# Performance work log

Hardware: AMD Instinct MI355X
Metric: run time of the kernel (lower is better)

The kernel has to match this reference:

```python
import jax, jax.numpy as jnp
import numpy as np

B, S, D, E, H, K = 2, 2048, 1024, 8, 4096, 2


def setup_inputs() -> dict:
    key = jax.random.key(0)
    ks = jax.random.split(key, 8)
    w = lambda i, shape: jax.random.normal(ks[i], shape, jnp.float32) * 0.02
    return {
        "x": jax.random.normal(ks[0], (B, S, D), jnp.float32),
        "noise": jax.random.normal(ks[1], (B, S, E), jnp.float32),
        "Wg": w(2, (E, D)),
        "noise_weight": jnp.zeros((E,), jnp.float32),
        "W1": w(3, (E, D, H)),
        "b1": jnp.zeros((E, H), jnp.float32),
        "W2": w(4, (E, D, H)),
        "b2": jnp.zeros((E, H), jnp.float32),
        "Wp": w(5, (E, H, D)),
        "bp": jnp.zeros((E, D), jnp.float32),
        "k": K,
    }


def reference(x, noise, Wg, noise_weight, W1, b1, W2, b2, Wp, bp, k):
    Bb, Ss, Dd = x.shape
    Ee = Wg.shape[0]
    # --- noisy top-k gate (noisy_std = 1.0) ---
    logits = jnp.einsum('bsd,ed->bse', x, Wg)
    noisy = logits + noise * noise_weight            # [B,S,E]
    vals, idx = jax.lax.top_k(noisy, k)              # [B,S,k]
    oh = jax.nn.one_hot(idx, Ee, dtype=x.dtype)      # [B,S,k,E]
    sel = oh.sum(axis=-2) > 0                        # [B,S,E] selected mask
    scat = (oh * vals[..., None]).sum(axis=-2)       # scatter topk logits
    sparse = jnp.where(sel, scat, -jnp.inf)
    gate = jax.nn.softmax(sparse, axis=-1)           # zero weight off-topk
    # --- dense-equivalent expert compute (gate==0 off top-k => same math as masked dispatch) ---
    xf = x.reshape(Bb * Ss, Dd)                      # [T,D]
    gf = gate.reshape(Bb * Ss, Ee)                   # [T,E]
    h1 = jnp.einsum('td,edh->eth', xf, W1) + b1[:, None, :]
    h2 = jnp.einsum('td,edh->eth', xf, W2) + b2[:, None, :]
    hh = h1 * jax.nn.silu(h2)                        # SwiGLU
    outs = jnp.einsum('eth,ehd->etd', hh, Wp) + bp[:, None, :]
    final = jnp.einsum('etd,te->td', outs, gf).reshape(Bb, Ss, Dd)
    return final, idx
```

## Files before the change

kernel.cpp:

```cpp
#include <hip/hip_runtime.h>
#include <math.h>

#define Bc 2
#define Sc 2048
#define Dc 1024
#define Ec 8
#define Hc 4096
#define Tc (Bc*Sc)
#define NSLOT (Tc*2)
#define SLOTPAD 8448
#define FINAL_N ((size_t)Tc*Dc)
#define PROWS ((size_t)SLOTPAD*32)

typedef float f32x4 __attribute__((ext_vector_type(4)));
typedef __bf16 bf16x8 __attribute__((ext_vector_type(8)));

__device__ __forceinline__ unsigned short f2bf(float f) {
    union { float f; unsigned int u; } v; v.f = f;
    return (unsigned short)((v.u + 0x7fffu + ((v.u >> 16) & 1u)) >> 16);
}
__device__ __forceinline__ unsigned int pack2bf(float a, float b) {
    return (unsigned int)f2bf(a) | ((unsigned int)f2bf(b) << 16);
}

__device__ __forceinline__ void gload16(const unsigned short* g, unsigned short* l) {
    __builtin_amdgcn_global_load_lds(
        (const __attribute__((address_space(1))) unsigned int*)g,
        (__attribute__((address_space(3))) unsigned int*)l,
        16, 0, 0);
}

__device__ __forceinline__ void fence_bar() {
    __builtin_amdgcn_sched_barrier(0);
    asm volatile("s_barrier" ::: "memory");
    __builtin_amdgcn_sched_barrier(0);
}

__global__ void k_transpose_panel(const float* __restrict__ inA, const float* __restrict__ inB,
                                  unsigned short* __restrict__ outA, unsigned short* __restrict__ outB,
                                  int R, int C, int nz_per_mat) {
    __shared__ float tile[64][65];
    int z = blockIdx.z;
    const float* in; unsigned short* out;
    if (z < nz_per_mat) { in = inA; out = outA; }
    else { in = inB; out = outB; z -= nz_per_mat; }
    size_t zbase = (size_t)z * (size_t)R * C;
    int R32 = R >> 5;
    int cb = blockIdx.x * 64, rb = blockIdx.y * 64;
    int t = threadIdx.x;
    int q = t & 15, g = t >> 4;
    #pragma unroll
    for (int j = 0; j < 4; j++) {
        int row = g + 16*j;
        float4 v = *(const float4*)&in[zbase + (size_t)(rb+row)*C + cb + q*4];
        tile[row][q*4+0] = v.x; tile[row][q*4+1] = v.y;
        tile[row][q*4+2] = v.z; tile[row][q*4+3] = v.w;
    }
    __syncthreads();
    #pragma unroll
    for (int j = 0; j < 4; j++) {
        int co = g + 16*j;
        int c = cb + co;
        int r0 = rb + q*4;
        ushort4 o;
        o.x = f2bf(tile[q*4+0][co]); o.y = f2bf(tile[q*4+1][co]);
        o.z = f2bf(tile[q*4+2][co]); o.w = f2bf(tile[q*4+3][co]);
        int cr = c & 127;
        int ch = ((r0 >> 3) & 3) ^ ((cr >> 1) & 3);
        size_t off = zbase + (((size_t)(c >> 7) * R32 + (r0 >> 5)) * 4096)
                   + (size_t)cr * 32 + ch * 8 + (r0 & 7);
        *(ushort4*)&out[off] = o;
    }
}

__global__ void k_gate(const float* __restrict__ x, const float* __restrict__ noise,
                       const float* __restrict__ Wg, const float* __restrict__ nw,
                       float* __restrict__ out_idx, int* __restrict__ counts,
                       int* __restrict__ tok_top, float* __restrict__ tok_w) {
    int t = blockIdx.x;
    int lane = threadIdx.x;
    const float* xr = x + (size_t)t * Dc;
    double acc[Ec];
    #pragma unroll
    for (int e = 0; e < Ec; e++) acc[e] = 0.0;
    for (int i = 0; i < Dc/64; i++) {
        int d = lane + i*64;
        double xv = (double)xr[d];
        #pragma unroll
        for (int e = 0; e < Ec; e++) acc[e] += xv * (double)Wg[e*Dc + d];
    }
    #pragma unroll
    for (int e = 0; e < Ec; e++)
        for (int off = 32; off > 0; off >>= 1)
            acc[e] += __shfl_down(acc[e], off);
    if (lane == 0) {
        double noisy[Ec];
        #pragma unroll
        for (int e = 0; e < Ec; e++)
            noisy[e] = acc[e] + (double)noise[t*Ec + e] * (double)nw[e];
        int i0 = 0;
        for (int e = 1; e < Ec; e++) if (noisy[e] > noisy[i0]) i0 = e;
        int i1 = -1;
        for (int e = 0; e < Ec; e++) {
            if (e == i0) continue;
            if (i1 < 0 || noisy[e] > noisy[i1]) i1 = e;
        }
        double ee = exp(noisy[i1] - noisy[i0]);
        float w0 = (float)(1.0 / (1.0 + ee));
        float w1 = (float)(ee / (1.0 + ee));
        out_idx[t*2 + 0] = (float)i0;
        out_idx[t*2 + 1] = (float)i1;
        tok_top[t*2] = i0; tok_top[t*2+1] = i1;
        tok_w[t*2] = w0;   tok_w[t*2+1] = w1;
        atomicAdd(&counts[i0], 1);
        atomicAdd(&counts[i1], 1);
    }
}

__global__ void k_scan(const int* __restrict__ counts, int* __restrict__ offsets) {
    if (threadIdx.x == 0) {
        int s = 0;
        for (int e = 0; e < Ec; e++) { offsets[e] = s; s += counts[e]; }
        offsets[Ec] = s;
    }
}

__global__ void k_fill(const int* __restrict__ tok_top, const int* __restrict__ offsets,
                       int* __restrict__ fill, int* __restrict__ slot_token,
                       int* __restrict__ slot_of, int* __restrict__ slot_pos) {
    int t = blockIdx.x * 256 + threadIdx.x;
    if (t >= Tc) return;
    #pragma unroll
    for (int j = 0; j < 2; j++) {
        int e = tok_top[t*2 + j];
        int pos = atomicAdd(&fill[e], 1);
        int slot = offsets[e] + pos;
        slot_token[slot] = t;
        slot_of[t*2 + j] = slot;
        slot_pos[slot] = pos;
    }
}

__global__ void k_packA(const float* __restrict__ x, const int* __restrict__ slot_token,
                        const int* __restrict__ slot_pos, unsigned short* __restrict__ apk) {
    int s = blockIdx.x * 4 + (threadIdx.x >> 6);
    int lane = threadIdx.x & 63;
    int token = slot_token[s];
    int pos = slot_pos[s];
    const float4* px = (const float4*)(x + (size_t)token * Dc) + lane*4;
    float4 v0 = px[0], v1 = px[1], v2 = px[2], v3 = px[3];
    uint4 lo, hi;
    lo.x = pack2bf(v0.x, v0.y); lo.y = pack2bf(v0.z, v0.w);
    lo.z = pack2bf(v1.x, v1.y); lo.w = pack2bf(v1.z, v1.w);
    hi.x = pack2bf(v2.x, v2.y); hi.y = pack2bf(v2.z, v2.w);
    hi.z = pack2bf(v3.x, v3.y); hi.w = pack2bf(v3.z, v3.w);
    int kp = lane >> 1;
    int key = (pos >> 1) & 3;
    int c0 = (lane & 1) * 2;
    size_t base = (size_t)kp * PROWS + (size_t)s * 32;
    *(uint4*)&apk[base + ((c0 ^ key) * 8)]       = lo;
    *(uint4*)&apk[base + (((c0+1) ^ key) * 8)]   = hi;
}

__global__ __launch_bounds__(256, 4) void k_gemm1(
    const unsigned short* __restrict__ apk,
    const unsigned short* __restrict__ w1p, const unsigned short* __restrict__ w2p,
    const float* __restrict__ b1, const float* __restrict__ b2,
    const int* __restrict__ counts, const int* __restrict__ offsets,
    unsigned short* __restrict__ hh2) {
    int e = blockIdx.z;
    int n_e = counts[e];
    int m0 = blockIdx.y * 128;
    if (m0 >= n_e) return;
    int base = offsets[e];
    int bx = blockIdx.x;
    int n0 = bx * 64;
    int hp = bx >> 1, ro = (bx & 1) * 64;

    __shared__ __align__(16) unsigned char smem[32768];
    unsigned short* sU = (unsigned short*)smem;
    float* sS = (float*)smem;

    int tid = threadIdx.x;
    int wid = tid >> 6, lane = tid & 63;
    int wr = wid >> 1, wc = wid & 1;

    const unsigned short* aSrc = apk + (size_t)(base + m0 + wid*32)*32 + lane*8;
    const unsigned short* wmat = (wid < 2) ? w1p : w2p;
    const unsigned short* bSrc = wmat + ((size_t)(e*32 + hp) * 32) * 4096
                               + (size_t)(ro + (wid & 1)*32)*32 + lane*8;

    int arow = lane & 15, cr = lane >> 4;
    int ccf = cr ^ ((arow >> 1) & 3);
    int aoff[4], boff[4];
    #pragma unroll
    for (int m = 0; m < 4; m++) aoff[m] = (wr*64 + m*16 + arow)*32 + ccf*8;
    #pragma unroll
    for (int n = 0; n < 4; n++) boff[n] = 8192 + (wc*64 + n*16 + arow)*32 + ccf*8;

    f32x4 acc[4][4];
    #pragma unroll
    for (int m = 0; m < 4; m++)
        #pragma unroll
        for (int n = 0; n < 4; n++)
            #pragma unroll
            for (int j = 0; j < 4; j++) acc[m][n][j] = 0.0f;

    auto STAGE = [&](int s, int kk) {
        const unsigned short* a = aSrc + (size_t)kk*PROWS;
        const unsigned short* b = bSrc + (size_t)kk*4096;
        unsigned short* dA = sU + s*4096 + wid*1024;
        unsigned short* dB = sU + 8192 + s*4096 + wid*1024;
        gload16(a,       dA); gload16(a + 512, dA + 512);
        gload16(b,       dB); gload16(b + 512, dB + 512);
    };

    const int NK = Dc / 32;
    STAGE(0, 0); STAGE(1, 1);
    for (int kk = 0; kk < NK; ++kk) {
        int s = kk & 1;
        const unsigned short* sl = sU + s*4096;
        if (kk < NK - 1) { asm volatile("s_waitcnt vmcnt(4)" ::: "memory"); }
        else             { asm volatile("s_waitcnt vmcnt(0)" ::: "memory"); }
        fence_bar();
        bf16x8 af[4], bf[4];
        #pragma unroll
        for (int m = 0; m < 4; m++) af[m] = *(const bf16x8*)&sl[aoff[m]];
        #pragma unroll
        for (int n = 0; n < 4; n++) bf[n] = *(const bf16x8*)&sl[boff[n]];
        #pragma unroll
        for (int m = 0; m < 4; m++)
            #pragma unroll
            for (int n = 0; n < 4; n++)
                acc[m][n] = __builtin_amdgcn_mfma_f32_16x16x32_bf16(af[m], bf[n], acc[m][n], 0, 0, 0);
        fence_bar();
        if (kk + 2 < NK) STAGE(s, kk + 2);
    }

    int lrow = (lane >> 4) * 4, lcol = lane & 15;
    if (wc == 1) {
        #pragma unroll
        for (int n = 0; n < 4; n++) {
            float b2v = b2[e*Hc + n0 + n*16 + lcol];
            #pragma unroll
            for (int m = 0; m < 4; m++) {
                int rb = wr*64 + m*16 + lrow;
                #pragma unroll
                for (int j = 0; j < 4; j++) {
                    float h2 = acc[m][n][j] + b2v;
                    sS[(rb + j)*64 + ((n*16 + lcol) ^ (j << 4))] = h2 / (1.0f + expf(-h2));
                }
            }
        }
    }
    __syncthreads();
    if (wc == 0) {
        #pragma unroll
        for (int n = 0; n < 4; n++) {
            int hcol = n0 + n*16 + lcol;
            float b1v = b1[e*Hc + hcol];
            int hp2 = hcol >> 5;
            int ch  = (hcol >> 3) & 3;
            int ho  = hcol & 7;
            #pragma unroll
            for (int m = 0; m < 4; m++) {
                int rb = wr*64 + m*16 + lrow;
                #pragma unroll
                for (int j = 0; j < 4; j++) {
                    int r = m0 + rb + j;
                    if (r < n_e) {
                        float v = (acc[m][n][j] + b1v) * sS[(rb + j)*64 + ((n*16 + lcol) ^ (j << 4))];
                        int key = (r >> 1) & 3;
                        hh2[(size_t)hp2 * PROWS + (size_t)(base + r)*32 + ((ch ^ key)*8) + ho] = f2bf(v);
                    }
                }
            }
        }
    }
}

__global__ __launch_bounds__(256, 4) void k_gemm2(
    const unsigned short* __restrict__ hh2,
    const unsigned short* __restrict__ wpp,
    const float* __restrict__ bp,
    const int* __restrict__ counts, const int* __restrict__ offsets,
    float* __restrict__ outb) {
    int e = blockIdx.z;
    int n_e = counts[e];
    int m0 = blockIdx.y * 128;
    if (m0 >= n_e) return;
    int base = offsets[e];
    int dp = blockIdx.x;
    int n0 = dp * 128;

    __shared__ __align__(16) unsigned char smem[32768];
    unsigned short* sU = (unsigned short*)smem;

    int tid = threadIdx.x;
    int wid = tid >> 6, lane = tid & 63;
    int wr = wid >> 1, wc = wid & 1;

    const unsigned short* aSrc = hh2 + (size_t)(base + m0 + wid*32)*32 + lane*8;
    const unsigned short* bSrc = wpp + ((size_t)(e*8 + dp) * 128) * 4096
                               + wid*1024 + lane*8;

    int arow = lane & 15, cr = lane >> 4;
    int ccf = cr ^ ((arow >> 1) & 3);
    int aoff[4], boff[4];
    #pragma unroll
    for (int m = 0; m < 4; m++) aoff[m] = (wr*64 + m*16 + arow)*32 + ccf*8;
    #pragma unroll
    for (int n = 0; n < 4; n++) boff[n] = 8192 + (wc*64 + n*16 + arow)*32 + ccf*8;

    f32x4 acc[4][4];
    #pragma unroll
    for (int m = 0; m < 4; m++)
        #pragma unroll
        for (int n = 0; n < 4; n++)
            #pragma unroll
            for (int j = 0; j < 4; j++) acc[m][n][j] = 0.0f;

    auto STAGE = [&](int s, int kk) {
        const unsigned short* a = aSrc + (size_t)kk*PROWS;
        const unsigned short* b = bSrc + (size_t)kk*4096;
        unsigned short* dA = sU + s*4096 + wid*1024;
        unsigned short* dB = sU + 8192 + s*4096 + wid*1024;
        gload16(a,       dA); gload16(a + 512, dA + 512);
        gload16(b,       dB); gload16(b + 512, dB + 512);
    };

    const int NK = Hc / 32;
    STAGE(0, 0); STAGE(1, 1);
    for (int kk = 0; kk < NK; ++kk) {
        int s = kk & 1;
        const unsigned short* sl = sU + s*4096;
        if (kk < NK - 1) { asm volatile("s_waitcnt vmcnt(4)" ::: "memory"); }
        else             { asm volatile("s_waitcnt vmcnt(0)" ::: "memory"); }
        fence_bar();
        bf16x8 af[4], bf[4];
        #pragma unroll
        for (int m = 0; m < 4; m++) af[m] = *(const bf16x8*)&sl[aoff[m]];
        #pragma unroll
        for (int n = 0; n < 4; n++) bf[n] = *(const bf16x8*)&sl[boff[n]];
        #pragma unroll
        for (int m = 0; m < 4; m++)
            #pragma unroll
            for (int n = 0; n < 4; n++)
                acc[m][n] = __builtin_amdgcn_mfma_f32_16x16x32_bf16(af[m], bf[n], acc[m][n], 0, 0, 0);
        fence_bar();
        if (kk + 2 < NK) STAGE(s, kk + 2);
    }

    int lrow = (lane >> 4) * 4, lcol = lane & 15;
    #pragma unroll
    for (int n = 0; n < 4; n++) {
        int dcol = n0 + wc*64 + n*16 + lcol;
        float bias = bp[e*Dc + dcol];
        #pragma unroll
        for (int m = 0; m < 4; m++) {
            int rb2 = m0 + wr*64 + m*16 + lrow;
            #pragma unroll
            for (int j = 0; j < 4; j++) {
                int r = rb2 + j;
                if (r < n_e)
                    outb[(size_t)(base + r)*Dc + dcol] = acc[m][n][j] + bias;
            }
        }
    }
}

__global__ void k_combine(const float* __restrict__ outb, const int* __restrict__ slot_of,
                          const float* __restrict__ tok_w, float* __restrict__ final_out) {
    int gid = blockIdx.x * 256 + threadIdx.x;
    int t = gid >> 8;
    int c = (gid & 255) * 4;
    int s0 = slot_of[t*2], s1 = slot_of[t*2 + 1];
    float w0 = tok_w[t*2], w1 = tok_w[t*2 + 1];
    float4 o0 = *(const float4*)&outb[(size_t)s0*Dc + c];
    float4 o1 = *(const float4*)&outb[(size_t)s1*Dc + c];
    float4 r;
    r.x = w0*o0.x + w1*o1.x;
    r.y = w0*o0.y + w1*o1.y;
    r.z = w0*o0.z + w1*o1.z;
    r.w = w0*o0.w + w1*o1.w;
    *(float4*)&final_out[(size_t)t*Dc + c] = r;
}

extern "C" void kernel_launch(void* const* d_in, const int* in_sizes, int n_in,
                              void* d_out, int out_size, void* d_ws, size_t ws_size,
                              hipStream_t stream) {
    (void)in_sizes; (void)n_in; (void)out_size; (void)ws_size;
    const float* x     = (const float*)d_in[0];
    const float* noise = (const float*)d_in[1];
    const float* Wg    = (const float*)d_in[2];
    const float* nw    = (const float*)d_in[3];
    const float* W1    = (const float*)d_in[4];
    const float* b1    = (const float*)d_in[5];
    const float* W2    = (const float*)d_in[6];
    const float* b2    = (const float*)d_in[7];
    const float* Wp    = (const float*)d_in[8];
    const float* bp    = (const float*)d_in[9];

    char* ws = (char*)d_ws;
    size_t off = 0;
    unsigned short* W1P = (unsigned short*)(ws + off); off += (size_t)Ec*Dc*Hc*2;
    unsigned short* W2P = (unsigned short*)(ws + off); off += (size_t)Ec*Dc*Hc*2;
    unsigned short* WPP = (unsigned short*)(ws + off); off += (size_t)Ec*Hc*Dc*2;
    unsigned short* APK = (unsigned short*)(ws + off); off += (size_t)32*PROWS*2;
    unsigned short* HH2 = (unsigned short*)(ws + off); off += (size_t)128*PROWS*2;
    float*          OUTB= (float*)(ws + off);          off += (size_t)NSLOT*Dc*4;
    int*   counts    = (int*)(ws + off);
    int*   fill      = (int*)(ws + off + 32);
    int*   offsets   = (int*)(ws + off + 64);
    int*   tok_top   = (int*)(ws + off + 128);
    float* tok_w     = (float*)(ws + off + 128 + (size_t)Tc*2*4);
    int*   slot_token= (int*)(ws + off + 128 + (size_t)Tc*2*8);
    int*   slot_of   = (int*)(ws + off + 128 + (size_t)Tc*2*8 + (size_t)NSLOT*4);
    int*   slot_pos  = (int*)(ws + off + 128 + (size_t)Tc*2*8 + (size_t)NSLOT*8);

    float* final_out = (float*)d_out;
    float* idx_out   = (float*)d_out + FINAL_N;

    (void)hipMemsetAsync(counts, 0, 64, stream);

    k_transpose_panel<<<dim3(Hc/64, Dc/64, 2*Ec), 256, 0, stream>>>(W1, W2, W1P, W2P, Dc, Hc, Ec);
    k_transpose_panel<<<dim3(Dc/64, Hc/64, Ec), 256, 0, stream>>>(Wp, Wp, WPP, WPP, Hc, Dc, Ec);

    k_gate<<<Tc, 64, 0, stream>>>(x, noise, Wg, nw, idx_out, counts, tok_top, tok_w);
    k_scan<<<1, 64, 0, stream>>>(counts, offsets);
    k_fill<<<Tc/256, 256, 0, stream>>>(tok_top, offsets, fill, slot_token, slot_of, slot_pos);
    k_packA<<<NSLOT/4, 256, 0, stream>>>(x, slot_token, slot_pos, APK);

    k_gemm1<<<dim3(Hc/64, Tc/128, Ec), 256, 0, stream>>>(APK, W1P, W2P, b1, b2,
                                                         counts, offsets, HH2);
    k_gemm2<<<dim3(Dc/128, Tc/128, Ec), 256, 0, stream>>>(HH2, WPP, bp, counts, offsets, OUTB);
    k_combine<<<(Tc*Dc/4)/256, 256, 0, stream>>>(OUTB, slot_of, tok_w, final_out);
}
```

Measured before the change: 645.9 us.

## Split-K the second expert GEMM with atomic accumulation and tweak shared swizzle

The down-projection GEMM is split into two K halves, which doubles the grid. Each half accumulates into a zeroed output buffer with float atomicAdd, and only the first half adds the bias. Staging pointers are now advanced incrementally, and the gate GEMM's shared-memory swizzle for the SiLU tile changes to depend on the row. The aim is more blocks and better occupancy for the long-K GEMM, at the cost of an extra memset, atomic traffic, and a nondeterministic summation order.

```diff
diff --git a/kernel.cpp b/kernel.cpp
--- a/kernel.cpp
+++ b/kernel.cpp
@@ -206,17 +206,19 @@
             #pragma unroll
             for (int j = 0; j < 4; j++) acc[m][n][j] = 0.0f;
 
-    auto STAGE = [&](int s, int kk) {
-        const unsigned short* a = aSrc + (size_t)kk*PROWS;
-        const unsigned short* b = bSrc + (size_t)kk*4096;
+    const unsigned short* aStage = aSrc;
+    const unsigned short* bStage = bSrc;
+
+    auto STAGE = [&](int s) {
         unsigned short* dA = sU + s*4096 + wid*1024;
         unsigned short* dB = sU + 8192 + s*4096 + wid*1024;
-        gload16(a,       dA); gload16(a + 512, dA + 512);
-        gload16(b,       dB); gload16(b + 512, dB + 512);
+        gload16(aStage,       dA); gload16(aStage + 512, dA + 512);
+        gload16(bStage,       dB); gload16(bStage + 512, dB + 512);
+        aStage += PROWS; bStage += 4096;
     };
 
     const int NK = Dc / 32;
-    STAGE(0, 0); STAGE(1, 1);
+    STAGE(0); STAGE(1);
     for (int kk = 0; kk < NK; ++kk) {
         int s = kk & 1;
         const unsigned short* sl = sU + s*4096;
@@ -234,7 +236,7 @@
             for (int n = 0; n < 4; n++)
                 acc[m][n] = __builtin_amdgcn_mfma_f32_16x16x32_bf16(af[m], bf[n], acc[m][n], 0, 0, 0);
         fence_bar();
-        if (kk + 2 < NK) STAGE(s, kk + 2);
+        if (kk + 2 < NK) STAGE(s);
     }
 
     int lrow = (lane >> 4) * 4, lcol = lane & 15;
@@ -247,8 +249,9 @@
                 int rb = wr*64 + m*16 + lrow;
                 #pragma unroll
                 for (int j = 0; j < 4; j++) {
+                    int row = rb + j;
                     float h2 = acc[m][n][j] + b2v;
-                    sS[(rb + j)*64 + ((n*16 + lcol) ^ (j << 4))] = h2 / (1.0f + expf(-h2));
+                    sS[row*64 + ((n*16 + lcol) ^ ((((row) >> 2) & 1) << 4))] = h2 / (1.0f + expf(-h2));
                 }
             }
         }
@@ -267,9 +270,11 @@
                 int rb = wr*64 + m*16 + lrow;
                 #pragma unroll
                 for (int j = 0; j < 4; j++) {
-                    int r = m0 + rb + j;
+                    int row = rb + j;
+                    int r = m0 + row;
                     if (r < n_e) {
-                        float v = (acc[m][n][j] + b1v) * sS[(rb + j)*64 + ((n*16 + lcol) ^ (j << 4))];
+                        float sv = sS[row*64 + ((n*16 + lcol) ^ ((((row) >> 2) & 1) << 4))];
+                        float v = (acc[m][n][j] + b1v) * sv;
                         int key = (r >> 1) & 3;
                         hh2[(size_t)hp2 * PROWS + (size_t)(base + r)*32 + ((ch ^ key)*8) + ho] = f2bf(v);
                     }
@@ -287,7 +292,9 @@
     float* __restrict__ outb) {
     int e = blockIdx.z;
     int n_e = counts[e];
-    int m0 = blockIdx.y * 128;
+    int yy = blockIdx.y;
+    int kc = yy & 1;
+    int m0 = (yy >> 1) * 128;
     if (m0 >= n_e) return;
     int base = offsets[e];
     int dp = blockIdx.x;
@@ -300,9 +307,11 @@
     int wid = tid >> 6, lane = tid & 63;
     int wr = wid >> 1, wc = wid & 1;
 
-    const unsigned short* aSrc = hh2 + (size_t)(base + m0 + wid*32)*32 + lane*8;
+    const int k0 = kc * 64;
+    const unsigned short* aSrc = hh2 + (size_t)k0*PROWS
+                               + (size_t)(base + m0 + wid*32)*32 + lane*8;
     const unsigned short* bSrc = wpp + ((size_t)(e*8 + dp) * 128) * 4096
-                               + wid*1024 + lane*8;
+                               + (size_t)k0*4096 + wid*1024 + lane*8;
 
     int arow = lane & 15, cr = lane >> 4;
     int ccf = cr ^ ((arow >> 1) & 3);
@@ -320,17 +329,18 @@
             #pragma unroll
             for (int j = 0; j < 4; j++) acc[m][n][j] = 0.0f;
 
-    auto STAGE = [&](int s, int kk) {
-        const unsigned short* a = aSrc + (size_t)kk*PROWS;
-        const unsigned short* b = bSrc + (size_t)kk*4096;
+    const unsigned short* aStage = aSrc;
+    const unsigned short* bStage = bSrc;
+    auto STAGE = [&](int s) {
         unsigned short* dA = sU + s*4096 + wid*1024;
         unsigned short* dB = sU + 8192 + s*4096 + wid*1024;
-        gload16(a,       dA); gload16(a + 512, dA + 512);
-        gload16(b,       dB); gload16(b + 512, dB + 512);
+        gload16(aStage,       dA); gload16(aStage + 512, dA + 512);
+        gload16(bStage,       dB); gload16(bStage + 512, dB + 512);
+        aStage += PROWS; bStage += 4096;
     };
 
-    const int NK = Hc / 32;
-    STAGE(0, 0); STAGE(1, 1);
+    const int NK = 64;
+    STAGE(0); STAGE(1);
     for (int kk = 0; kk < NK; ++kk) {
         int s = kk & 1;
         const unsigned short* sl = sU + s*4096;
@@ -348,14 +358,14 @@
             for (int n = 0; n < 4; n++)
                 acc[m][n] = __builtin_amdgcn_mfma_f32_16x16x32_bf16(af[m], bf[n], acc[m][n], 0, 0, 0);
         fence_bar();
-        if (kk + 2 < NK) STAGE(s, kk + 2);
+        if (kk + 2 < NK) STAGE(s);
     }
 
     int lrow = (lane >> 4) * 4, lcol = lane & 15;
     #pragma unroll
     for (int n = 0; n < 4; n++) {
         int dcol = n0 + wc*64 + n*16 + lcol;
-        float bias = bp[e*Dc + dcol];
+        float badd = (kc == 0) ? bp[e*Dc + dcol] : 0.0f;
         #pragma unroll
         for (int m = 0; m < 4; m++) {
             int rb2 = m0 + wr*64 + m*16 + lrow;
@@ -363,7 +373,7 @@
             for (int j = 0; j < 4; j++) {
                 int r = rb2 + j;
                 if (r < n_e)
-                    outb[(size_t)(base + r)*Dc + dcol] = acc[m][n][j] + bias;
+                    atomicAdd(&outb[(size_t)(base + r)*Dc + dcol], acc[m][n][j] + badd);
             }
         }
     }
@@ -422,6 +432,7 @@
     float* idx_out   = (float*)d_out + FINAL_N;
 
     (void)hipMemsetAsync(counts, 0, 64, stream);
+    (void)hipMemsetAsync(OUTB, 0, (size_t)NSLOT*Dc*4, stream);
 
     k_transpose_panel<<<dim3(Hc/64, Dc/64, 2*Ec), 256, 0, stream>>>(W1, W2, W1P, W2P, Dc, Hc, Ec);
     k_transpose_panel<<<dim3(Dc/64, Hc/64, Ec), 256, 0, stream>>>(Wp, Wp, WPP, WPP, Hc, Dc, Ec);
@@ -433,6 +444,7 @@
 
     k_gemm1<<<dim3(Hc/64, Tc/128, Ec), 256, 0, stream>>>(APK, W1P, W2P, b1, b2,
                                                          counts, offsets, HH2);
-    k_gemm2<<<dim3(Dc/128, Tc/128, Ec), 256, 0, stream>>>(HH2, WPP, bp, counts, offsets, OUTB);
+    k_gemm2<<<dim3(Dc/128, (Tc/128)*2, Ec), 256, 0, stream>>>(HH2, WPP, bp,
+                                                              counts, offsets, OUTB);
     k_combine<<<(Tc*Dc/4)/256, 256, 0, stream>>>(OUTB, slot_of, tok_w, final_out);
 }
```

Result: slower. 672.9 us (+4.2%).
